# Performance work log

Hardware: AMD Instinct MI355X
Metric: run time of the kernel (lower is better)

Reference implementation:

```python
import jax, jax.numpy as jnp
import numpy as np

B, S, D, M, HID, THETA = 8, 4096, 128, 256, 256, 4096


def _impulse_response():
    """Build discretized LTI (A,B) via ZOH and the impulse response H [M, S]."""
    Q = jnp.arange(M, dtype=jnp.float32).reshape(-1, 1)          # [M,1]
    R = (2.0 * Q + 1.0) / THETA                                   # [M,1]
    ii, jj = jnp.meshgrid(jnp.arange(M), jnp.arange(M), indexing='ij')
    # (-1)^(i-j+1): -1 when (i-j) even, +1 when odd
    sign = jnp.where((ii - jj) % 2 == 0, -1.0, 1.0)
    A = R * jnp.where(ii < jj, -1.0, sign)                        # [M,M]
    Bv = R * jnp.where(jnp.arange(M).reshape(-1, 1) % 2 == 0, 1.0, -1.0)  # [M,1]
    # zero-order-hold discretization via matrix exponential of augmented system
    aug = jnp.zeros((M + 1, M + 1), dtype=jnp.float32)
    aug = aug.at[:M, :M].set(A).at[:M, M].set(Bv[:, 0])
    expA = jax.scipy.linalg.expm(aug)
    Ad, Bd = expA[:M, :M], expA[:M, M:M + 1]
    # H[:, i] = Ad^i @ Bd
    def step(Ai, _):
        return Ad @ Ai, (Ai @ Bd)[:, 0]
    _, Hs = jax.lax.scan(step, jnp.eye(M, dtype=jnp.float32), None, length=S)
    return Hs.T  # [M, S]


def setup_inputs() -> dict:
    key = jax.random.key(0)
    k1, k2, k3 = jax.random.split(key, 3)
    x = jax.random.normal(k1, (B, S, D), dtype=jnp.float32)
    W_u = jax.random.normal(k2, (D, 1), dtype=jnp.float32) / np.sqrt(D)
    b_u = jnp.zeros((1,), dtype=jnp.float32)
    W_h = jax.random.normal(k3, (M + D, HID), dtype=jnp.float32) / np.sqrt(M + D)
    b_h = jnp.zeros((HID,), dtype=jnp.float32)
    H = _impulse_response()  # [M, S], fixed (non-trainable) impulse response
    return {"x": x, "W_u": W_u, "b_u": b_u, "W_h": W_h, "b_h": b_h, "H": H}


def reference(x, W_u, b_u, W_h, b_h, H):
    batch, seq_len, _ = x.shape
    n = 2 * seq_len
    # u_t = relu(W_u x_t)  -> [B, S, 1]
    u = jax.nn.relu(jnp.einsum('bsd,do->bso', x, W_u) + b_u)
    fft_H = jnp.fft.rfft(H, n=n, axis=-1)                 # [M, S+1]
    fft_u = jnp.fft.rfft(u[..., 0], n=n, axis=-1)         # [B, S+1]
    temp = fft_u[:, None, :] * fft_H[None, :, :]          # [B, M, S+1] complex
    m = jnp.fft.irfft(temp, n=n, axis=-1)[:, :, :seq_len]  # [B, M, S]
    m = jnp.transpose(m, (0, 2, 1))                       # [B, S, M]
    input_h = jnp.concatenate([m, x], axis=-1)            # [B, S, M+D]
    h = jax.nn.relu(jnp.einsum('bsf,fh->bsh', input_h, W_h) + b_h)
    h_n = h[:, -1, :]
    return (h, h_n)
```

## Files before the change

kernel.cpp:

```cpp
#include <hip/hip_runtime.h>

#define S_LEN 4096
#define B_SZ 8
#define HN_OFF 8388608
#define CPROWS 544

typedef __attribute__((ext_vector_type(8))) short short8;
typedef __attribute__((ext_vector_type(4))) float f32x4;

typedef const __attribute__((address_space(1))) unsigned int as1_u32;
typedef __attribute__((address_space(3))) unsigned int as3_u32;

__device__ __forceinline__ void gload16(const short* g, short* l) {
  __builtin_amdgcn_global_load_lds((as1_u32*)g, (as3_u32*)l, 16, 0, 0);
}

__device__ __forceinline__ short f2bf(float f) {
  union { float f; unsigned u; } v; v.f = f;
  unsigned r = v.u + 0x7FFFu + ((v.u >> 16) & 1u);
  return (short)(r >> 16);
}

#define MFMA(d, a, bb) d = __builtin_amdgcn_mfma_f32_16x16x32_bf16(a, bb, d, 0, 0, 0)

__global__ __launch_bounds__(256) void k_prep(const float* __restrict__ x,
                                              const float* __restrict__ Wu,
                                              const float* __restrict__ bu,
                                              const float* __restrict__ H,
                                              const float* __restrict__ Wh,
                                              short* __restrict__ cp,
                                              short* __restrict__ xb,
                                              short* __restrict__ Ht,
                                              short* __restrict__ wht) {
  int bx = blockIdx.x;
  if (bx >= 8520) {
    int j = (bx - 8520) * 256 + threadIdx.x;
    if (j < 256 * 384) {
      int n = j / 384, k = j % 384;
      wht[j] = f2bf(Wh[k * 256 + n]);
    }
    return;
  }
  if (bx >= 8264) {
    __shared__ short tile[64][72];
    int bx2 = bx - 8264;
    int t0 = (bx2 >> 2) << 6, q0 = (bx2 & 3) << 6;
    int tid = threadIdx.x;
    int r = tid >> 2, c0 = (tid & 3) << 4;
    const float* src = H + (size_t)(q0 + r) * S_LEN + t0 + c0;
    #pragma unroll
    for (int v4 = 0; v4 < 4; ++v4) {
      float4 hv = *(const float4*)(src + 4 * v4);
      tile[r][c0 + 4 * v4]     = f2bf(hv.x);
      tile[r][c0 + 4 * v4 + 1] = f2bf(hv.y);
      tile[r][c0 + 4 * v4 + 2] = f2bf(hv.z);
      tile[r][c0 + 4 * v4 + 3] = f2bf(hv.w);
    }
    __syncthreads();
    int s2 = tid >> 2, qc = (tid & 3) << 4;
    short8 o0, o1;
    #pragma unroll
    for (int j2 = 0; j2 < 8; ++j2) {
      o0[j2] = tile[qc + j2][s2];
      o1[j2] = tile[qc + 8 + j2][s2];
    }
    short* dst = Ht + (size_t)(t0 + s2) * 256 + q0 + qc;
    *(short8*)dst       = o0;
    *(short8*)(dst + 8) = o1;
    return;
  }
  if (bx >= 8192) {
    int idx = (bx - 8192) * 256 + threadIdx.x;
    if (idx < 18432) {
      int j = idx & 7;
      int r = 508 + ((idx >> 3) % 36);
      int rem = (idx >> 3) / 36;
      int p = rem & 7;
      int b = rem >> 3;
      int e = 8 * r + p + j;
      if (e >= S_LEN)
        cp[((size_t)(b * 8 + p) * CPROWS + r) * 8 + j] = 0;
    }
    return;
  }
  int row = bx * 4 + (threadIdx.x >> 6);
  int l = threadIdx.x & 63;
  float2 xv = *(const float2*)(x + (size_t)row * 128 + 2 * l);
  float2 wv = *(const float2*)(Wu + 2 * l);
  float s = xv.x * wv.x + xv.y * wv.y;
  #pragma unroll
  for (int m = 32; m >= 1; m >>= 1) s += __shfl_xor(s, m, 64);
  unsigned pack = (((unsigned)f2bf(xv.y) & 0xFFFFu) << 16) | ((unsigned)f2bf(xv.x) & 0xFFFFu);
  *(unsigned*)(xb + (size_t)row * 128 + 2 * l) = pack;
  float v = s + bu[0];
  v = v > 0.0f ? v : 0.0f;
  short vb = f2bf(v);
  if (l < 8) {
    int t = row & (S_LEN - 1);
    int b = row >> 12;
    int e = (S_LEN - 1) - t;
    int p = l;
    if (e >= p) {
      int d = e - p;
      cp[((size_t)(b * 8 + p) * CPROWS + (d >> 3)) * 8 + (d & 7)] = vb;
    }
  }
}

__global__ __launch_bounds__(256) void k_g(const short* __restrict__ wht,
                                           const short* __restrict__ Ht,
                                           short* __restrict__ Gt) {
  int nt = blockIdx.x & 1, tt = blockIdx.x >> 1;
  int n0 = nt << 7, t0 = tt << 7;
  int tid = threadIdx.x;
  int lane = tid & 63, wid = tid >> 6;
  int wr = wid >> 1, wc = wid & 1;
  int lm = lane & 15, kg = lane >> 4;

  const short* Abase = wht + (size_t)(n0 + wr * 64 + lm) * 384 + 8 * kg;
  const short* Bbase = Ht  + (size_t)(t0 + wc * 64 + lm) * 256 + 8 * kg;

  f32x4 acc[4][4];
  #pragma unroll
  for (int ii = 0; ii < 4; ++ii)
    #pragma unroll
    for (int jn = 0; jn < 4; ++jn)
      acc[ii][jn] = (f32x4){0.0f, 0.0f, 0.0f, 0.0f};

  #pragma unroll
  for (int c = 0; c < 4; ++c) {
    short8 a[8], bf[8];
    #pragma unroll
    for (int mf = 0; mf < 4; ++mf)
      #pragma unroll
      for (int ks = 0; ks < 2; ++ks)
        a[mf * 2 + ks] = *(const short8*)(Abase + mf * 16 * 384 + c * 64 + ks * 32);
    #pragma unroll
    for (int nf = 0; nf < 4; ++nf)
      #pragma unroll
      for (int ks = 0; ks < 2; ++ks)
        bf[nf * 2 + ks] = *(const short8*)(Bbase + nf * 16 * 256 + c * 64 + ks * 32);
    #pragma unroll
    for (int ks = 0; ks < 2; ++ks)
      #pragma unroll
      for (int mf = 0; mf < 4; ++mf)
        #pragma unroll
        for (int nf = 0; nf < 4; ++nf)
          MFMA(acc[mf][nf], a[mf * 2 + ks], bf[nf * 2 + ks]);
  }

  #pragma unroll
  for (int mf = 0; mf < 4; ++mf)
    #pragma unroll
    for (int nf = 0; nf < 4; ++nf)
      #pragma unroll
      for (int j = 0; j < 4; ++j) {
        int n = n0 + wr * 64 + mf * 16 + kg * 4 + j;
        int t = t0 + wc * 64 + nf * 16 + lm;
        Gt[(size_t)n * S_LEN + t] = f2bf(acc[mf][nf][j]);
      }
}

__global__ __launch_bounds__(256, 2) void k_fused(const short* __restrict__ cp,
                                                  const short* __restrict__ Gt,
                                                  const short* __restrict__ xb,
                                                  const short* __restrict__ wht,
                                                  const float* __restrict__ bh,
                                                  float* __restrict__ out) {
  __shared__ __attribute__((aligned(16))) short Bt[4][64 * 128];
  __shared__ __attribute__((aligned(16))) short Aw[4][2048];

  int i = blockIdx.x;
  int kk = i >> 5;
  int nq = (i >> 3) & 3;
  int b  = i & 7;
  int n0 = nq << 6;

  int tid = threadIdx.x;
  int lane = tid & 63, wid = tid >> 6;
  int wr = wid >> 1, wc = wid & 1;
  int lm = lane & 15, kg = lane >> 4;
  int l3 = lane >> 3, l7 = lane & 7;
  int lm7 = lm & 7;

  const short* bS0 = Gt + (size_t)(n0 + wid * 16 + kg) * S_LEN + ((lm ^ kg) << 3);
  const short* bS1 = Gt + (size_t)(n0 + wid * 16 + 4 + kg) * S_LEN + ((lm ^ (kg | 4)) << 3);

  int dbase = 127 - 64 * wr - lm + 8 * kg;
  int aof[10];
  #pragma unroll
  for (int v = 0; v < 10; ++v) {
    int d = dbase + 16 * v - 48;
    aof[v] = ((d & ~7) | ((d & 7) ^ ((d >> 3) & 7))) << 3;
  }

  int bof[8];
  #pragma unroll
  for (int nf = 0; nf < 2; ++nf)
    #pragma unroll
    for (int ks = 0; ks < 4; ++ks)
      bof[nf * 4 + ks] = (wc * 32 + nf * 16 + lm) * 128 + (((4 * ks + kg) ^ lm7) << 3);

  int xof[4][2];
  #pragma unroll
  for (int mf = 0; mf < 4; ++mf)
    #pragma unroll
    for (int ks = 0; ks < 2; ++ks)
      xof[mf][ks] = (wr * 64 + mf * 16 + lm) * 64 + (((4 * ks + kg) ^ lm7) << 3);

  for (int ph = 0; ph < 2; ++ph) {
    int st = ph ? kk : (31 - kk);
    int s0 = st << 7;
    int asbase = 496 - 16 * st;
    const short* aSrc = cp + ((size_t)(b * 8 + (l7 ^ l3)) * CPROWS + asbase + wid * 8 + l3) * 8;
    const short* xS = xb + (size_t)(b * S_LEN + s0 + wid * 32 + l3) * 128 + ((l7 ^ l3) << 3);

    int NT = st + 1;
    int NC = NT + 2;

    f32x4 acc[4][2];
    #pragma unroll
    for (int ii = 0; ii < 4; ++ii)
      #pragma unroll
      for (int jn = 0; jn < 2; ++jn)
        acc[ii][jn] = (f32x4){0.0f, 0.0f, 0.0f, 0.0f};

    auto STAGE = [&](int cc) {
      int slot = cc & 3;
      if (cc < NT) {
        int coff = cc * 128;
        gload16(bS0 + coff,                      &Bt[slot][(wid * 16) * 128]);
        gload16(bS1 + coff,                      &Bt[slot][(wid * 16 + 4) * 128]);
        gload16(bS0 + (size_t)8 * S_LEN + coff,  &Bt[slot][(wid * 16 + 8) * 128]);
        gload16(bS1 + (size_t)8 * S_LEN + coff,  &Bt[slot][(wid * 16 + 12) * 128]);
        gload16(aSrc + coff,                     &Aw[slot][wid * 512]);
      } else {
        int dc = cc - NT;
        #pragma unroll
        for (int jj = 0; jj < 4; ++jj)
          gload16(xS + (size_t)(8 * jj) * 128 + dc * 64, &Bt[slot][(wid * 32 + 8 * jj) * 64]);
        gload16(aSrc, &Aw[slot][wid * 512]);
      }
    };

    if (ph) asm volatile("s_waitcnt vmcnt(0) lgkmcnt(0)\n\ts_barrier" ::: "memory");
    STAGE(0);
    STAGE(1);

    for (int c = 0; c < NC; ++c) {
      if (c + 2 < NC) {
        STAGE(c + 2);
        asm volatile("s_waitcnt vmcnt(10) lgkmcnt(0)\n\ts_barrier" ::: "memory");
      } else if (c + 1 < NC) {
        asm volatile("s_waitcnt vmcnt(5) lgkmcnt(0)\n\ts_barrier" ::: "memory");
      } else {
        asm volatile("s_waitcnt vmcnt(0) lgkmcnt(0)\n\ts_barrier" ::: "memory");
      }

      if (c < NT) {
        const short* AwB = &Aw[c & 3][0];
        const short* BtB = &Bt[c & 3][0];
        short8 A10[10];
        #pragma unroll
        for (int v = 0; v < 10; ++v) A10[v] = *(const short8*)(AwB + aof[v]);
        short8 Bf[8];
        #pragma unroll
        for (int ii = 0; ii < 8; ++ii) Bf[ii] = *(const short8*)(BtB + bof[ii]);
        __builtin_amdgcn_s_setprio(1);
        #pragma unroll
        for (int ks = 0; ks < 4; ++ks)
          #pragma unroll
          for (int mf = 0; mf < 4; ++mf)
            #pragma unroll
            for (int nf = 0; nf < 2; ++nf)
              MFMA(acc[mf][nf], A10[2 * ks - mf + 3], Bf[nf * 4 + ks]);
        __builtin_amdgcn_s_setprio(0);
      } else {
        int dc = c - NT;
        const short* BtB = &Bt[c & 3][0];
        short8 Ax[4][2];
        #pragma unroll
        for (int mf = 0; mf < 4; ++mf)
          #pragma unroll
          for (int ks = 0; ks < 2; ++ks)
            Ax[mf][ks] = *(const short8*)(BtB + xof[mf][ks]);
        short8 Bx[2][2];
        #pragma unroll
        for (int ks = 0; ks < 2; ++ks)
          #pragma unroll
          for (int nf = 0; nf < 2; ++nf)
            Bx[ks][nf] = *(const short8*)(wht + (size_t)(n0 + wc * 32 + nf * 16 + lm) * 384
                                          + 256 + dc * 64 + ks * 32 + kg * 8);
        __builtin_amdgcn_s_setprio(1);
        #pragma unroll
        for (int ks = 0; ks < 2; ++ks)
          #pragma unroll
          for (int mf = 0; mf < 4; ++mf)
            #pragma unroll
            for (int nf = 0; nf < 2; ++nf)
              MFMA(acc[mf][nf], Ax[mf][ks], Bx[ks][nf]);
        __builtin_amdgcn_s_setprio(0);
      }
    }

    #pragma unroll
    for (int mf = 0; mf < 4; ++mf)
      #pragma unroll
      for (int nf = 0; nf < 2; ++nf) {
        int n = n0 + wc * 32 + nf * 16 + lm;
        float bias = bh[n];
        #pragma unroll
        for (int j2 = 0; j2 < 4; ++j2) {
          int s = s0 + wr * 64 + mf * 16 + kg * 4 + j2;
          float v = acc[mf][nf][j2] + bias;
          v = v > 0.0f ? v : 0.0f;
          out[(size_t)(b * S_LEN + s) * 256 + n] = v;
          if (s == S_LEN - 1)
            out[HN_OFF + b * 256 + n] = v;
        }
      }
  }
}

extern "C" void kernel_launch(void* const* d_in, const int* in_sizes, int n_in,
                              void* d_out, int out_size, void* d_ws, size_t ws_size,
                              hipStream_t stream) {
  const float* x  = (const float*)d_in[0];
  const float* Wu = (const float*)d_in[1];
  const float* bu = (const float*)d_in[2];
  const float* Wh = (const float*)d_in[3];
  const float* bh = (const float*)d_in[4];
  const float* H  = (const float*)d_in[5];
  float* out = (float*)d_out;

  char* ws = (char*)d_ws;
  short* cp  = (short*)(ws);
  short* wht = (short*)(ws + 557056);
  short* xb  = (short*)(ws + 753664);
  short* Ht  = (short*)(ws + 9142272);
  short* Gt  = (short*)(ws + 11239424);

  k_prep<<<8904, 256, 0, stream>>>(x, Wu, bu, H, Wh, cp, xb, Ht, wht);
  k_g   <<<64,   256, 0, stream>>>(wht, Ht, Gt);
  k_fused<<<512, 256, 0, stream>>>(cp, Gt, xb, wht, bh, out);
}
```

Before: 67.12 us.

## Use two waves per block with 64x64 warp tiles and double buffering

Cuts k_fused from four waves (2x2 over a 128x64 tile) to two waves, each computing 64 rows by the full 64 columns. This doubles per-wave MFMA reuse of the Toeplitz A fragments and removes the duplicated A loads. The LDS ring drops from four stages to two, with a full wait-and-barrier every iteration, which shrinks LDS per block but exposes more load latency. Fewer waves per block also reduce latency hiding across the 512 blocks, and the launch bounds no longer request two blocks per CU.

Result: slower. 81.56 us (+21.5%).

```diff
diff --git a/kernel.cpp b/kernel.cpp
--- a/kernel.cpp
+++ b/kernel.cpp
@@ -161,14 +161,14 @@
       }
 }
 
-__global__ __launch_bounds__(256, 2) void k_fused(const short* __restrict__ cp,
-                                                  const short* __restrict__ Gt,
-                                                  const short* __restrict__ xb,
-                                                  const short* __restrict__ wht,
-                                                  const float* __restrict__ bh,
-                                                  float* __restrict__ out) {
-  __shared__ __attribute__((aligned(16))) short Bt[4][64 * 128];
-  __shared__ __attribute__((aligned(16))) short Aw[4][2048];
+__global__ __launch_bounds__(128) void k_fused(const short* __restrict__ cp,
+                                               const short* __restrict__ Gt,
+                                               const short* __restrict__ xb,
+                                               const short* __restrict__ wht,
+                                               const float* __restrict__ bh,
+                                               float* __restrict__ out) {
+  __shared__ __attribute__((aligned(16))) short Bt[2][64 * 128];
+  __shared__ __attribute__((aligned(16))) short Aw[2][2048];
 
   int i = blockIdx.x;
   int kk = i >> 5;
@@ -178,15 +178,14 @@
 
   int tid = threadIdx.x;
   int lane = tid & 63, wid = tid >> 6;
-  int wr = wid >> 1, wc = wid & 1;
   int lm = lane & 15, kg = lane >> 4;
   int l3 = lane >> 3, l7 = lane & 7;
   int lm7 = lm & 7;
 
-  const short* bS0 = Gt + (size_t)(n0 + wid * 16 + kg) * S_LEN + ((lm ^ kg) << 3);
-  const short* bS1 = Gt + (size_t)(n0 + wid * 16 + 4 + kg) * S_LEN + ((lm ^ (kg | 4)) << 3);
-
-  int dbase = 127 - 64 * wr - lm + 8 * kg;
+  const short* bSe = Gt + (size_t)(n0 + wid * 32 + kg) * S_LEN + ((lm ^ kg) << 3);
+  const short* bSo = Gt + (size_t)(n0 + wid * 32 + 4 + kg) * S_LEN + ((lm ^ (kg | 4)) << 3);
+
+  int dbase = 127 - 64 * wid - lm + 8 * kg;
   int aof[10];
   #pragma unroll
   for (int v = 0; v < 10; ++v) {
@@ -194,102 +193,101 @@
     aof[v] = ((d & ~7) | ((d & 7) ^ ((d >> 3) & 7))) << 3;
   }
 
-  int bof[8];
-  #pragma unroll
-  for (int nf = 0; nf < 2; ++nf)
+  int bof[4][4];
+  #pragma unroll
+  for (int nf = 0; nf < 4; ++nf)
     #pragma unroll
     for (int ks = 0; ks < 4; ++ks)
-      bof[nf * 4 + ks] = (wc * 32 + nf * 16 + lm) * 128 + (((4 * ks + kg) ^ lm7) << 3);
+      bof[nf][ks] = (nf * 16 + lm) * 128 + (((4 * ks + kg) ^ lm7) << 3);
 
   int xof[4][2];
   #pragma unroll
   for (int mf = 0; mf < 4; ++mf)
     #pragma unroll
     for (int ks = 0; ks < 2; ++ks)
-      xof[mf][ks] = (wr * 64 + mf * 16 + lm) * 64 + (((4 * ks + kg) ^ lm7) << 3);
+      xof[mf][ks] = (wid * 64 + mf * 16 + lm) * 64 + (((4 * ks + kg) ^ lm7) << 3);
 
   for (int ph = 0; ph < 2; ++ph) {
     int st = ph ? kk : (31 - kk);
     int s0 = st << 7;
     int asbase = 496 - 16 * st;
-    const short* aSrc = cp + ((size_t)(b * 8 + (l7 ^ l3)) * CPROWS + asbase + wid * 8 + l3) * 8;
-    const short* xS = xb + (size_t)(b * S_LEN + s0 + wid * 32 + l3) * 128 + ((l7 ^ l3) << 3);
+    const short* aSrc = cp + ((size_t)(b * 8 + (l7 ^ l3)) * CPROWS + asbase + wid * 16 + l3) * 8;
+    const short* xS = xb + (size_t)(b * S_LEN + s0 + wid * 64 + l3) * 128 + ((l7 ^ l3) << 3);
 
     int NT = st + 1;
     int NC = NT + 2;
 
-    f32x4 acc[4][2];
+    f32x4 acc[4][4];
     #pragma unroll
     for (int ii = 0; ii < 4; ++ii)
       #pragma unroll
-      for (int jn = 0; jn < 2; ++jn)
+      for (int jn = 0; jn < 4; ++jn)
         acc[ii][jn] = (f32x4){0.0f, 0.0f, 0.0f, 0.0f};
 
     auto STAGE = [&](int cc) {
-      int slot = cc & 3;
+      int slot = cc & 1;
       if (cc < NT) {
         int coff = cc * 128;
-        gload16(bS0 + coff,                      &Bt[slot][(wid * 16) * 128]);
-        gload16(bS1 + coff,                      &Bt[slot][(wid * 16 + 4) * 128]);
-        gload16(bS0 + (size_t)8 * S_LEN + coff,  &Bt[slot][(wid * 16 + 8) * 128]);
-        gload16(bS1 + (size_t)8 * S_LEN + coff,  &Bt[slot][(wid * 16 + 12) * 128]);
-        gload16(aSrc + coff,                     &Aw[slot][wid * 512]);
+        #pragma unroll
+        for (int j = 0; j < 4; ++j) {
+          gload16(bSe + (size_t)(8 * j) * S_LEN + coff, &Bt[slot][(wid * 32 + 8 * j) * 128]);
+          gload16(bSo + (size_t)(8 * j) * S_LEN + coff, &Bt[slot][(wid * 32 + 8 * j + 4) * 128]);
+        }
+        gload16(aSrc + coff,       &Aw[slot][(wid * 2) * 512]);
+        gload16(aSrc + 64 + coff,  &Aw[slot][(wid * 2 + 1) * 512]);
       } else {
         int dc = cc - NT;
         #pragma unroll
-        for (int jj = 0; jj < 4; ++jj)
-          gload16(xS + (size_t)(8 * jj) * 128 + dc * 64, &Bt[slot][(wid * 32 + 8 * jj) * 64]);
-        gload16(aSrc, &Aw[slot][wid * 512]);
+        for (int j = 0; j < 8; ++j)
+          gload16(xS + (size_t)(8 * j) * 128 + dc * 64, &Bt[slot][(wid * 64 + 8 * j) * 64]);
       }
     };
 
     if (ph) asm volatile("s_waitcnt vmcnt(0) lgkmcnt(0)\n\ts_barrier" ::: "memory");
     STAGE(0);
-    STAGE(1);
 
     for (int c = 0; c < NC; ++c) {
-      if (c + 2 < NC) {
-        STAGE(c + 2);
-        asm volatile("s_waitcnt vmcnt(10) lgkmcnt(0)\n\ts_barrier" ::: "memory");
-      } else if (c + 1 < NC) {
-        asm volatile("s_waitcnt vmcnt(5) lgkmcnt(0)\n\ts_barrier" ::: "memory");
-      } else {
-        asm volatile("s_waitcnt vmcnt(0) lgkmcnt(0)\n\ts_barrier" ::: "memory");
-      }
+      asm volatile("s_waitcnt vmcnt(0) lgkmcnt(0)\n\ts_barrier" ::: "memory");
+      if (c + 1 < NC) STAGE(c + 1);
 
       if (c < NT) {
-        const short* AwB = &Aw[c & 3][0];
-        const short* BtB = &Bt[c & 3][0];
+        const short* AwB = &Aw[c & 1][0];
+        const short* BtB = &Bt[c & 1][0];
         short8 A10[10];
         #pragma unroll
         for (int v = 0; v < 10; ++v) A10[v] = *(const short8*)(AwB + aof[v]);
-        short8 Bf[8];
-        #pragma unroll
-        for (int ii = 0; ii < 8; ++ii) Bf[ii] = *(const short8*)(BtB + bof[ii]);
         __builtin_amdgcn_s_setprio(1);
         #pragma unroll
-        for (int ks = 0; ks < 4; ++ks)
+        for (int ks = 0; ks < 4; ++ks) {
+          short8 B0 = *(const short8*)(BtB + bof[0][ks]);
+          short8 B1 = *(const short8*)(BtB + bof[1][ks]);
+          short8 B2 = *(const short8*)(BtB + bof[2][ks]);
+          short8 B3 = *(const short8*)(BtB + bof[3][ks]);
           #pragma unroll
-          for (int mf = 0; mf < 4; ++mf)
-            #pragma unroll
-            for (int nf = 0; nf < 2; ++nf)
-              MFMA(acc[mf][nf], A10[2 * ks - mf + 3], Bf[nf * 4 + ks]);
+          for (int mf = 0; mf < 4; ++mf) {
+            short8 a = A10[2 * ks - mf + 3];
+            MFMA(acc[mf][0], a, B0);
+            MFMA(acc[mf][1], a, B1);
+            MFMA(acc[mf][2], a, B2);
+            MFMA(acc[mf][3], a, B3);
+          }
+        }
         __builtin_amdgcn_s_setprio(0);
       } else {
         int dc = c - NT;
-        const short* BtB = &Bt[c & 3][0];
+        const short* BtB = &Bt[c & 1][0];
         short8 Ax[4][2];
         #pragma unroll
         for (int mf = 0; mf < 4; ++mf)
           #pragma unroll
           for (int ks = 0; ks < 2; ++ks)
             Ax[mf][ks] = *(const short8*)(BtB + xof[mf][ks]);
-        short8 Bx[2][2];
+        short8 Bx[2][4];
         #pragma unroll
         for (int ks = 0; ks < 2; ++ks)
           #pragma unroll
-          for (int nf = 0; nf < 2; ++nf)
-            Bx[ks][nf] = *(const short8*)(wht + (size_t)(n0 + wc * 32 + nf * 16 + lm) * 384
+          for (int nf = 0; nf < 4; ++nf)
+            Bx[ks][nf] = *(const short8*)(wht + (size_t)(n0 + nf * 16 + lm) * 384
                                           + 256 + dc * 64 + ks * 32 + kg * 8);
         __builtin_amdgcn_s_setprio(1);
         #pragma unroll
@@ -297,7 +295,7 @@
           #pragma unroll
           for (int mf = 0; mf < 4; ++mf)
             #pragma unroll
-            for (int nf = 0; nf < 2; ++nf)
+            for (int nf = 0; nf < 4; ++nf)
               MFMA(acc[mf][nf], Ax[mf][ks], Bx[ks][nf]);
         __builtin_amdgcn_s_setprio(0);
       }
@@ -306,12 +304,12 @@
     #pragma unroll
     for (int mf = 0; mf < 4; ++mf)
       #pragma unroll
-      for (int nf = 0; nf < 2; ++nf) {
-        int n = n0 + wc * 32 + nf * 16 + lm;
+      for (int nf = 0; nf < 4; ++nf) {
+        int n = n0 + nf * 16 + lm;
         float bias = bh[n];
         #pragma unroll
         for (int j2 = 0; j2 < 4; ++j2) {
-          int s = s0 + wr * 64 + mf * 16 + kg * 4 + j2;
+          int s = s0 + wid * 64 + mf * 16 + kg * 4 + j2;
           float v = acc[mf][nf][j2] + bias;
           v = v > 0.0f ? v : 0.0f;
           out[(size_t)(b * S_LEN + s) * 256 + n] = v;
@@ -342,5 +340,5 @@
 
   k_prep<<<8904, 256, 0, stream>>>(x, Wu, bu, H, Wh, cp, xb, Ht, wht);
   k_g   <<<64,   256, 0, stream>>>(wht, Ht, Gt);
-  k_fused<<<512, 256, 0, stream>>>(cp, Gt, xb, wht, bh, out);
-}
+  k_fused<<<512, 128, 0, stream>>>(cp, Gt, xb, wht, bh, out);
+}
```
